# Optimization experiments

Measured on AMD Instinct MI355X. Metric: run time of the kernel, lower is better.

## Reference

```python
import jax, jax.numpy as jnp
import numpy as np

STEP, LEAK = 16, 32
KS = STEP + LEAK          # kernel_size = 48
FODEP = KS                # forced depression window
SYNAPSES, NEURONS = 64, 256
IC, OC = 1, 10
DENSE = 0.5
THETA = DENSE * SYNAPSES * IC   # 32.0
BIAS = 0.5
BATCH, TIME = 16, 512


def setup_inputs() -> dict:
    key = jax.random.key(0)
    k1, k2 = jax.random.split(key)
    # binary input spikes, density 0.2
    input_spikes = (jax.random.uniform(k1, (BATCH, IC, SYNAPSES, TIME)) < 0.2).astype(jnp.float32)
    # weight ~ Exponential(rate=1/w_init=2).sample().clip(0,1), mean 0.5
    u = jax.random.uniform(k2, (OC * NEURONS, IC * SYNAPSES), minval=1e-6, maxval=1.0)
    weight = jnp.clip(-0.5 * jnp.log(u), 0.0, 1.0)
    return {"input_spikes": input_spikes, "weight": weight}


def _step_fire_leak_kernel(weight):
    # kernel[o, i, t] = max(0, min(t/step, -(t - w*step)/leak + w)), flipped on t
    t = jnp.arange(KS, dtype=weight.dtype)
    t_spike = t / STEP                                        # rising edge
    t_leak = -(t - weight[..., None] * STEP) / LEAK + weight[..., None]  # decaying edge
    kernel = jnp.maximum(jnp.zeros((), weight.dtype), jnp.minimum(t_spike, t_leak))
    return kernel[..., ::-1]


def _forward(input_spikes, weight):
    B, C, S, T = input_spikes.shape
    x = input_spikes.reshape(B, C * S, T)
    kernel = _step_fire_leak_kernel(weight)                   # [OC*N, IC*S, KS]
    # conv1d with padding = kernel_size on both sides -> T' = T + KS + 1
    pot = jax.lax.conv_general_dilated(
        x, kernel, window_strides=(1,), padding=[(KS, KS)],
        dimension_numbers=("NCH", "OIH", "NCH"))
    Tp = pot.shape[-1]
    pot = pot.reshape(B, OC, NEURONS, Tp) + BIAS * THETA      # unsupervised bias path

    # winner-takes-all scan over time with per-(batch, neuron) depression counter
    pot_t = pot.transpose(3, 0, 2, 1)                         # [T', B, N, OC]
    dep0 = jnp.zeros((B, NEURONS, OC), jnp.int32)

    def step_fn(dep, p):
        masked = jnp.where(dep == 0, p, jnp.zeros((), p.dtype))
        winner = jnp.argmax(masked, axis=-1)                  # [B, N]
        wpot = jnp.take_along_axis(masked, winner[..., None], axis=-1)[..., 0]
        spike = (wpot > THETA).astype(p.dtype)                # [B, N]
        w_t = jax.nn.one_hot(winner, OC, dtype=p.dtype) * spike[..., None]
        dep = jnp.clip(dep + spike.astype(jnp.int32)[..., None] * FODEP - 1, 0, FODEP - 1)
        return dep, w_t

    _, winners = jax.lax.scan(step_fn, dep0, pot_t)           # [T', B, N, OC]
    return winners.transpose(1, 3, 2, 0)                      # [B, OC, N, T'] float


def reference(input_spikes, weight):
    return _forward(input_spikes, weight)
```

## Files before the change

### kernel.cpp

```cpp
#include <hip/hip_runtime.h>

#define B_   16
#define OC_  10
#define N_   256
#define O_   2560
#define S_   64
#define T_   512
#define KS_  48
#define TP_  561
#define TT   24
#define WROW 72

#define NOC   160
#define XROWS 624

#define SCH    16
#define CPITCH 572

using i32x4 = __attribute__((ext_vector_type(4))) int;

__global__ void prep_all(const float* __restrict__ x, const float* __restrict__ w,
                         unsigned char* __restrict__ xb, signed char* __restrict__ Bg) {
    if (blockIdx.x < 2048) {
        int idx = blockIdx.x * 256 + threadIdx.x;
        int t = idx & 511;
        int bi = idx >> 9;
        int i = bi & 63, b = bi >> 6;
        xb[((size_t)(b * 512 + t) << 6) + i] = (x[idx] != 0.0f) ? 1 : 0;
    } else {
        int idx = (blockIdx.x - 2048) * 256 + threadIdx.x;
        int i = idx & 63;
        int oj = idx >> 6;
        int j = oj % KS_, o = oj / KS_;
        float wv = w[(o << 6) + i];
        float rise = (float)j * 0.0625f;
        float leak = -((float)j - wv * 16.0f) * 0.03125f + wv;
        float kv   = fmaxf(0.0f, fminf(rise, leak));
        int q  = (int)lrintf(kv * 4194304.0f);
        int d0 = ((q + 128) & 255) - 128;
        int q1 = (q - d0) >> 8;
        int d1 = ((q1 + 128) & 255) - 128;
        int d2 = (q1 - d1) >> 8;
        int oc = o >> 4, ol = o & 15;
        int jm = j & 15, jh = j >> 4;
        int pos = jm * 3 + jh;
        size_t base = (((size_t)(oc * KS_ + pos) * 48) + ol) * 64 + i;
        Bg[base]            = (signed char)d0;
        Bg[base + 16 * 64]  = (signed char)d1;
        Bg[base + 32 * 64]  = (signed char)d2;
    }
}

__global__ __launch_bounds__(256, 2) void gemm_i8(
    const unsigned char* __restrict__ xb,
    const signed char*  __restrict__ Bg,
    float* __restrict__ pot)
{
    __shared__ __align__(16) unsigned char xT[XROWS * 64];

    const int tid  = threadIdx.x;
    const int lane = tid & 63;
    const int wave = tid >> 6;
    const int oc = blockIdx.x;
    const int b  = blockIdx.y;
    const int lrow = lane & 15;
    const int quad = lane >> 4;
    const int tw = wave * 144;

    const signed char* Bgb = Bg + (size_t)oc * (KS_ * 48 * 64)
                           + lrow * 64 + quad * 16;

    for (int z = tid; z < 112 * 4; z += 256) {
        int zi = z >> 2, p = z & 3;
        int r = (zi < 49) ? zi : (561 + zi - 49);
        *(i32x4*)(xT + r * 64 + p * 16) = (i32x4){0, 0, 0, 0};
    }
    const unsigned char* xbb = xb + ((size_t)b << 15);
    for (int q = tid; q < 2048; q += 256) {
        i32x4 v = *(const i32x4*)(xbb + q * 16);
        int t = q >> 2, p = q & 3;
        int r = 49 + t;
        *(i32x4*)(xT + r * 64 + ((p ^ ((r >> 1) & 3)) << 4)) = v;
    }

    i32x4 acc[9][3];
#pragma unroll
    for (int mi = 0; mi < 9; ++mi)
#pragma unroll
        for (int f = 0; f < 3; ++f)
            acc[mi][f] = (i32x4){0, 0, 0, 0};

    i32x4 bfA[9], bfB[9];

    auto loadB = [&](int t, i32x4 (&d)[9]) {
#pragma unroll
        for (int jh = 0; jh < 3; ++jh)
#pragma unroll
            for (int f = 0; f < 3; ++f)
                d[jh * 3 + f] = *(const i32x4*)(Bgb + (t * 3 + jh) * 3072 + f * 1024);
    };

    auto tlocBody = [&](int t, const i32x4 (&bf)[9]) {
        const int rb = tw + 16 - t + lrow;
        const int coffA = ((quad ^ ((rb >> 1) & 3)) << 4);
        i32x4 af[11];
#pragma unroll
        for (int k = 0; k < 11; ++k)
            af[k] = *(const i32x4*)(xT + (rb + k * 16) * 64 + coffA);
        __builtin_amdgcn_s_setprio(1);
#pragma unroll
        for (int jh = 0; jh < 3; ++jh)
#pragma unroll
            for (int mi = 0; mi < 9; ++mi)
#pragma unroll
                for (int f = 0; f < 3; ++f)
                    acc[mi][f] = __builtin_amdgcn_mfma_i32_16x16x64_i8(
                        af[mi + 2 - jh], bf[jh * 3 + f], acc[mi][f], 0, 0, 0);
        __builtin_amdgcn_s_setprio(0);
    };

    __syncthreads();

    loadB(0, bfA);
    for (int tp = 0; tp < 8; ++tp) {
        loadB(2 * tp + 1, bfB);
        tlocBody(2 * tp, bfA);
        if (tp < 7) loadB(2 * tp + 2, bfA);
        tlocBody(2 * tp + 1, bfB);
    }

    const size_t potb = (size_t)b * TP_;
#pragma unroll
    for (int mi = 0; mi < 9; ++mi) {
#pragma unroll
        for (int r = 0; r < 4; ++r) {
            int t = tw + mi * 16 + quad * 4 + r;
            if (t < TP_) {
                double pq = ((double)acc[mi][0][r]
                           + 256.0   * (double)acc[mi][1][r]
                           + 65536.0 * (double)acc[mi][2][r])
                          * (1.0 / 4194304.0);
                pot[(potb + t) * O_ + oc * 16 + lrow] = (float)pq;
            }
        }
    }
}

__global__ __launch_bounds__(1024) void scan_fused(
    const float* __restrict__ pot,
    float* __restrict__ out)
{
    __shared__ unsigned char codeW[SCH * CPITCH];
    __shared__ unsigned char ocW[SCH * CPITCH];

    const int tid = threadIdx.x;
    const int nc = blockIdx.x;
    const int b  = blockIdx.y;
    const int n0 = nc * SCH;

    for (int pair = tid; pair < TP_ * SCH; pair += 1024) {
        int t = pair >> 4, nl = pair & 15;
        const float* p = pot + ((size_t)(b * TP_ + t)) * O_ + n0 + nl;
        float best = p[0]; int bo = 0;
#pragma unroll
        for (int ch = 1; ch < OC_; ++ch) {
            float v = p[ch * N_];
            if (v > best) { best = v; bo = ch; }
        }
        codeW[nl * CPITCH + t] =
            ((best + 16.0f) > 32.0f) ? (unsigned char)(bo + 1) : (unsigned char)0;
        ocW[nl * CPITCH + t] = 0;
    }
    __syncthreads();

    if (tid < SCH) {
        const unsigned char* c = &codeW[tid * CPITCH];
        unsigned char* o = &ocW[tid * CPITCH];
        int t = 0;
        while (t < TP_) {
            unsigned char buf[KS_];
#pragma unroll
            for (int k = 0; k < KS_; ++k) {
                int tt = t + k;
                buf[k] = (tt < TP_) ? c[tt] : (unsigned char)0;
            }
            int adv = KS_;
#pragma unroll
            for (int k = 0; k < KS_; ++k) {
                if (buf[k]) { o[t + k] = buf[k]; adv = k + KS_; break; }
            }
            t += adv;
        }
    }
    __syncthreads();

    float* ob = out + (((size_t)b * OC_) * N_ + n0) * TP_;
    for (int idx = tid; idx < OC_ * SCH * TP_; idx += 1024) {
        int r = idx / TP_;
        int t = idx - r * TP_;
        int ch = r >> 4, nl = r & 15;
        float v = (ocW[nl * CPITCH + t] == (unsigned char)(ch + 1)) ? 1.0f : 0.0f;
        ob[((size_t)ch * N_ + nl) * TP_ + t] = v;
    }
}

__global__ void transpose_w(const float* __restrict__ w, float* __restrict__ wT) {
    int idx = blockIdx.x * 256 + threadIdx.x;
    if (idx >= O_ * S_) return;
    int o = idx >> 6, i = idx & 63;
    wT[i * O_ + o] = w[idx];
}

__global__ __launch_bounds__(256) void conv_kernel(
    const float* __restrict__ x, const float* __restrict__ wT,
    float* __restrict__ pot)
{
    const int b  = blockIdx.y;
    const int t0 = blockIdx.z * TT;
    const int o  = blockIdx.x * 256 + threadIdx.x;

    __shared__ __align__(16) float xsh[S_][WROW];
    for (int idx = threadIdx.x; idx < S_ * WROW; idx += 256) {
        int i = idx / WROW, m = idx - i * WROW;
        int t = t0 - KS_ + m;
        float v = 0.0f;
        if (t >= 0 && t < T_) v = x[(b * S_ + i) * T_ + t];
        xsh[i][m] = v;
    }
    __syncthreads();

    float acch[TT], accl[TT];
#pragma unroll
    for (int tl = 0; tl < TT; ++tl) { acch[tl] = 0.0f; accl[tl] = 0.0f; }

    for (int i = 0; i < S_; ++i) {
        float xw[WROW];
#pragma unroll
        for (int w4 = 0; w4 < WROW / 4; ++w4) {
            const float4 v = *reinterpret_cast<const float4*>(&xsh[i][w4 * 4]);
            xw[w4 * 4 + 0] = v.x; xw[w4 * 4 + 1] = v.y;
            xw[w4 * 4 + 2] = v.z; xw[w4 * 4 + 3] = v.w;
        }
        const float wv = wT[i * O_ + o];
#pragma unroll
        for (int j = 1; j < KS_; ++j) {
            float rise = (float)j * 0.0625f;
            float leak = -((float)j - wv * 16.0f) * 0.03125f + wv;
            float kv   = fmaxf(0.0f, fminf(rise, leak));
            float khi  = rintf(kv * 4096.0f) * 2.44140625e-4f;
            float klo  = kv - khi;
#pragma unroll
            for (int tl = 0; tl < TT; ++tl) {
                float xv = xw[tl + (KS_ - 1) - j];
                acch[tl] = fmaf(xv, khi, acch[tl]);
                accl[tl] = fmaf(xv, klo, accl[tl]);
            }
        }
    }
#pragma unroll
    for (int tl = 0; tl < TT; ++tl) {
        int t = t0 + tl;
        if (t < TP_) pot[((size_t)b * TP_ + t) * O_ + o] = acch[tl] + accl[tl];
    }
}

__global__ void scan_prep(const float* __restrict__ pot, unsigned char* __restrict__ code) {
    int idx = blockIdx.x * 256 + threadIdx.x;
    if (idx >= B_ * TP_ * N_) return;
    int n  = idx & (N_ - 1);
    int bt = idx >> 8;
    const float* p = pot + (size_t)bt * O_ + n;
    float best = p[0]; int bo = 0;
#pragma unroll
    for (int oc = 1; oc < OC_; ++oc) {
        float v = p[oc * N_];
        if (v > best) { best = v; bo = oc; }
    }
    code[idx] = ((best + 16.0f) > 32.0f) ? (unsigned char)(bo + 1) : (unsigned char)0;
}

__global__ void scan_run(const unsigned char* __restrict__ code, float* __restrict__ out) {
    int idx = blockIdx.x * 256 + threadIdx.x;
    if (idx >= B_ * N_) return;
    int b = idx >> 8, n = idx & 255;
    const unsigned char* c = code + (size_t)b * TP_ * N_ + n;
    int t = 0;
    while (t < TP_) {
        unsigned char buf[KS_];
#pragma unroll
        for (int k = 0; k < KS_; ++k) {
            int tt = t + k;
            buf[k] = (tt < TP_) ? c[(size_t)tt * N_] : (unsigned char)0;
        }
        int adv = KS_;
#pragma unroll
        for (int k = 0; k < KS_; ++k) {
            if (buf[k]) {
                out[(((size_t)b * OC_ + (buf[k] - 1)) * N_ + n) * TP_ + (t + k)] = 1.0f;
                adv = k + KS_;
                break;
            }
        }
        t += adv;
    }
}

extern "C" void kernel_launch(void* const* d_in, const int* in_sizes, int n_in,
                              void* d_out, int out_size, void* d_ws, size_t ws_size,
                              hipStream_t stream) {
    const float* x = (const float*)d_in[0];
    const float* w = (const float*)d_in[1];
    float* out = (float*)d_out;

    char* ws = (char*)d_ws;
    const size_t szX = (size_t)B_ * T_ * S_;
    const size_t szB = (size_t)NOC * KS_ * 48 * 64;
    const size_t szP = (size_t)B_ * TP_ * O_ * 4;
    const size_t szC = (size_t)B_ * TP_ * N_;
    const size_t need = szX + szB + szP + szC;

    if (ws_size >= need) {
        unsigned char* xb  = (unsigned char*)ws;
        signed char* Bg    = (signed char*)(ws + szX);
        float* pot         = (float*)(ws + szX + szB);

        prep_all<<<2048 + 30720, 256, 0, stream>>>(x, w, xb, Bg);
        gemm_i8<<<dim3(NOC, B_), 256, 0, stream>>>(xb, Bg, pot);
        scan_fused<<<dim3(N_ / SCH, B_), 1024, 0, stream>>>(pot, out);
    } else {
        size_t pot_bytes  = (size_t)B_ * TP_ * O_ * sizeof(float);
        size_t code_bytes = (size_t)B_ * TP_ * N_;
        float* pot = (float*)ws;
        unsigned char* code = (unsigned char*)(ws + pot_bytes);
        float* wT = (float*)(ws + pot_bytes + code_bytes);

        hipMemsetAsync(d_out, 0, (size_t)out_size * sizeof(float), stream);
        transpose_w<<<(O_ * S_ + 255) / 256, 256, 0, stream>>>(w, wT);
        conv_kernel<<<dim3(O_ / 256, B_, (TP_ + TT - 1) / TT), 256, 0, stream>>>(x, wT, pot);
        scan_prep<<<(B_ * TP_ * N_ + 255) / 256, 256, 0, stream>>>(pot, code);
        scan_run<<<(B_ * N_ + 255) / 256, 256, 0, stream>>>(code, out);
    }
}
```

Baseline: 258.4 us.

## Interleave next-step LDS and weight loads with MFMA chains; coarsen prep grid

The int8 GEMM inner loop is restructured so that the A-fragment LDS reads and B-fragment global loads for the next time offset are issued between groups of MFMAs of the current offset, using macros in place of lambdas. The goal is to hide load latency behind matrix work instead of loading all A fragments up front for each step. Separately, the prep kernel now does 4 or 16 elements per thread with a much smaller grid, which cuts block launch overhead. The wrap at t=15 loads unused data for index 16 mod 16, which costs one wasted load set, and the interleaving may raise register pressure under launch_bounds(256,2).

```diff
diff --git a/kernel.cpp b/kernel.cpp
--- a/kernel.cpp
+++ b/kernel.cpp
@@ -21,33 +21,40 @@
 
 __global__ void prep_all(const float* __restrict__ x, const float* __restrict__ w,
                          unsigned char* __restrict__ xb, signed char* __restrict__ Bg) {
-    if (blockIdx.x < 2048) {
-        int idx = blockIdx.x * 256 + threadIdx.x;
-        int t = idx & 511;
-        int bi = idx >> 9;
-        int i = bi & 63, b = bi >> 6;
-        xb[((size_t)(b * 512 + t) << 6) + i] = (x[idx] != 0.0f) ? 1 : 0;
+    if (blockIdx.x < 512) {
+#pragma unroll
+        for (int it = 0; it < 4; ++it) {
+            int idx = blockIdx.x * 256 + threadIdx.x + it * 131072;
+            int t = idx & 511;
+            int bi = idx >> 9;
+            int i = bi & 63, b = bi >> 6;
+            xb[((size_t)(b * 512 + t) << 6) + i] = (x[idx] != 0.0f) ? 1 : 0;
+        }
     } else {
-        int idx = (blockIdx.x - 2048) * 256 + threadIdx.x;
-        int i = idx & 63;
-        int oj = idx >> 6;
-        int j = oj % KS_, o = oj / KS_;
-        float wv = w[(o << 6) + i];
-        float rise = (float)j * 0.0625f;
-        float leak = -((float)j - wv * 16.0f) * 0.03125f + wv;
-        float kv   = fmaxf(0.0f, fminf(rise, leak));
-        int q  = (int)lrintf(kv * 4194304.0f);
-        int d0 = ((q + 128) & 255) - 128;
-        int q1 = (q - d0) >> 8;
-        int d1 = ((q1 + 128) & 255) - 128;
-        int d2 = (q1 - d1) >> 8;
-        int oc = o >> 4, ol = o & 15;
-        int jm = j & 15, jh = j >> 4;
-        int pos = jm * 3 + jh;
-        size_t base = (((size_t)(oc * KS_ + pos) * 48) + ol) * 64 + i;
-        Bg[base]            = (signed char)d0;
-        Bg[base + 16 * 64]  = (signed char)d1;
-        Bg[base + 32 * 64]  = (signed char)d2;
+        int base = (blockIdx.x - 512) * 256 + threadIdx.x;
+#pragma unroll
+        for (int it = 0; it < 16; ++it) {
+            int idx = base + it * 491520;
+            int i = idx & 63;
+            int oj = idx >> 6;
+            int j = oj % KS_, o = oj / KS_;
+            float wv = w[(o << 6) + i];
+            float rise = (float)j * 0.0625f;
+            float leak = -((float)j - wv * 16.0f) * 0.03125f + wv;
+            float kv   = fmaxf(0.0f, fminf(rise, leak));
+            int q  = (int)lrintf(kv * 4194304.0f);
+            int d0 = ((q + 128) & 255) - 128;
+            int q1 = (q - d0) >> 8;
+            int d1 = ((q1 + 128) & 255) - 128;
+            int d2 = (q1 - d1) >> 8;
+            int oc = o >> 4, ol = o & 15;
+            int jm = j & 15, jh = j >> 4;
+            int pos = jm * 3 + jh;
+            size_t bse = (((size_t)(oc * KS_ + pos) * 48) + ol) * 64 + i;
+            Bg[bse]            = (signed char)d0;
+            Bg[bse + 16 * 64]  = (signed char)d1;
+            Bg[bse + 32 * 64]  = (signed char)d2;
+        }
     }
 }
 
@@ -90,44 +97,77 @@
         for (int f = 0; f < 3; ++f)
             acc[mi][f] = (i32x4){0, 0, 0, 0};
 
-    i32x4 bfA[9], bfB[9];
-
-    auto loadB = [&](int t, i32x4 (&d)[9]) {
-#pragma unroll
-        for (int jh = 0; jh < 3; ++jh)
-#pragma unroll
-            for (int f = 0; f < 3; ++f)
-                d[jh * 3 + f] = *(const i32x4*)(Bgb + (t * 3 + jh) * 3072 + f * 1024);
-    };
-
-    auto tlocBody = [&](int t, const i32x4 (&bf)[9]) {
-        const int rb = tw + 16 - t + lrow;
-        const int coffA = ((quad ^ ((rb >> 1) & 3)) << 4);
-        i32x4 af[11];
+    i32x4 af[11], bfA[9], bfB[9];
+
+#pragma unroll
+    for (int jh = 0; jh < 3; ++jh)
+#pragma unroll
+        for (int f = 0; f < 3; ++f)
+            bfA[jh * 3 + f] = *(const i32x4*)(Bgb + jh * 3072 + f * 1024);
+
+    __syncthreads();
+
+    {
+        const int rb0 = tw + 16 + lrow;
+        const int ca0 = ((quad ^ ((rb0 >> 1) & 3)) << 4);
 #pragma unroll
         for (int k = 0; k < 11; ++k)
-            af[k] = *(const i32x4*)(xT + (rb + k * 16) * 64 + coffA);
-        __builtin_amdgcn_s_setprio(1);
-#pragma unroll
-        for (int jh = 0; jh < 3; ++jh)
-#pragma unroll
-            for (int mi = 0; mi < 9; ++mi)
-#pragma unroll
-                for (int f = 0; f < 3; ++f)
-                    acc[mi][f] = __builtin_amdgcn_mfma_i32_16x16x64_i8(
-                        af[mi + 2 - jh], bf[jh * 3 + f], acc[mi][f], 0, 0, 0);
-        __builtin_amdgcn_s_setprio(0);
-    };
-
-    __syncthreads();
-
-    loadB(0, bfA);
+            af[k] = *(const i32x4*)(xT + (rb0 + k * 16) * 64 + ca0);
+    }
+
+#define MF(bfC, mi, jh, f)                                                    \
+    acc[mi][f] = __builtin_amdgcn_mfma_i32_16x16x64_i8(                       \
+        af[(mi) + 2 - (jh)], bfC[(jh) * 3 + (f)], acc[mi][f], 0, 0, 0)
+
+#define PAIR(bfC, m0)                                                         \
+    MF(bfC, m0, 0, 0); MF(bfC, m0, 0, 1); MF(bfC, m0, 0, 2);                  \
+    MF(bfC, (m0)+1, 0, 0); MF(bfC, (m0)+1, 0, 1); MF(bfC, (m0)+1, 0, 2);      \
+    MF(bfC, m0, 1, 0); MF(bfC, m0, 1, 1); MF(bfC, m0, 1, 2);                  \
+    MF(bfC, (m0)+1, 1, 0); MF(bfC, (m0)+1, 1, 1); MF(bfC, (m0)+1, 1, 2);      \
+    MF(bfC, m0, 2, 0); MF(bfC, m0, 2, 1); MF(bfC, m0, 2, 2);                  \
+    MF(bfC, (m0)+1, 2, 0); MF(bfC, (m0)+1, 2, 1); MF(bfC, (m0)+1, 2, 2);
+
+#define PAIR9(bfC)                                                            \
+    MF(bfC, 8, 0, 0); MF(bfC, 8, 0, 1); MF(bfC, 8, 0, 2);                     \
+    MF(bfC, 8, 1, 0); MF(bfC, 8, 1, 1); MF(bfC, 8, 1, 2);                     \
+    MF(bfC, 8, 2, 0); MF(bfC, 8, 2, 1); MF(bfC, 8, 2, 2);
+
+#define LDA_(row) (*(const i32x4*)(xT + (row) * 64 + coffN))
+#define LDB_(jh, f) (*(const i32x4*)(Bgb + (tn3 + (jh)) * 3072 + (f) * 1024))
+
+#define TLOC(T, bfC, bfN) {                                                   \
+        const int rbn   = tw + 16 - ((T) + 1) + lrow;    \
+        const int coffN = ((quad ^ ((rbn >> 1) & 3)) << 4);                   \
+        const int tn3   = (((T) + 1) & 15) * 3;         \
+        __builtin_amdgcn_s_setprio(1);                                        \
+        PAIR(bfC, 0)                                                          \
+        af[0] = LDA_(rbn);        af[1] = LDA_(rbn + 16);                     \
+        bfN[0] = LDB_(0, 0); bfN[1] = LDB_(0, 1); bfN[2] = LDB_(0, 2);        \
+        PAIR(bfC, 2)                                                          \
+        af[2] = LDA_(rbn + 32);   af[3] = LDA_(rbn + 48);                     \
+        bfN[3] = LDB_(1, 0); bfN[4] = LDB_(1, 1); bfN[5] = LDB_(1, 2);        \
+        PAIR(bfC, 4)                                                          \
+        af[4] = LDA_(rbn + 64);   af[5] = LDA_(rbn + 80);                     \
+        bfN[6] = LDB_(2, 0); bfN[7] = LDB_(2, 1); bfN[8] = LDB_(2, 2);        \
+        PAIR(bfC, 6)                                                          \
+        af[6] = LDA_(rbn + 96);   af[7] = LDA_(rbn + 112);                    \
+        PAIR9(bfC)                                                            \
+        af[8] = LDA_(rbn + 128);  af[9] = LDA_(rbn + 144);                    \
+        af[10] = LDA_(rbn + 160);                                             \
+        __builtin_amdgcn_s_setprio(0);                                        \
+    }
+
     for (int tp = 0; tp < 8; ++tp) {
-        loadB(2 * tp + 1, bfB);
-        tlocBody(2 * tp, bfA);
-        if (tp < 7) loadB(2 * tp + 2, bfA);
-        tlocBody(2 * tp + 1, bfB);
-    }
+        TLOC(2 * tp,     bfA, bfB)
+        TLOC(2 * tp + 1, bfB, bfA)
+    }
+
+#undef MF
+#undef PAIR
+#undef PAIR9
+#undef LDA_
+#undef LDB_
+#undef TLOC
 
     const size_t potb = (size_t)b * TP_;
 #pragma unroll
@@ -324,7 +364,7 @@
         signed char* Bg    = (signed char*)(ws + szX);
         float* pot         = (float*)(ws + szX + szB);
 
-        prep_all<<<2048 + 30720, 256, 0, stream>>>(x, w, xb, Bg);
+        prep_all<<<2432, 256, 0, stream>>>(x, w, xb, Bg);
         gemm_i8<<<dim3(NOC, B_), 256, 0, stream>>>(xb, Bg, pot);
         scan_fused<<<dim3(N_ / SCH, B_), 1024, 0, stream>>>(pot, out);
     } else {
```

Result: no change. 256.0 us (-0.9%).
